# Kernel optimization log

Hardware: AMD Instinct MI355X
Metric: run time of the kernel (lower is better)

Reference implementation:

```python
import jax, jax.numpy as jnp
import numpy as np

N_NODES = 100000
N_EDGES = 3200000
IN_DIM = 64
HID_DIM = 128
OUT_DIM = 2


def setup_inputs() -> dict:
    key = jax.random.key(0)
    k1, k2, k3, k4, k5, k6 = jax.random.split(key, 6)
    x = jax.random.normal(k1, (N_NODES, IN_DIM), dtype=jnp.float32)
    edge_index = jax.random.randint(k2, (2, N_EDGES), 0, N_NODES, dtype=jnp.int64)
    W_gcn = jax.random.normal(k3, (IN_DIM, HID_DIM), dtype=jnp.float32) / np.sqrt(IN_DIM)
    b_gcn = jax.random.normal(k4, (HID_DIM,), dtype=jnp.float32) * 0.02
    W_lin = jax.random.normal(k5, (HID_DIM, OUT_DIM), dtype=jnp.float32) / np.sqrt(HID_DIM)
    b_lin = jax.random.normal(k6, (OUT_DIM,), dtype=jnp.float32) * 0.02
    return {"x": x, "edge_index": edge_index, "W_gcn": W_gcn, "b_gcn": b_gcn,
            "W_lin": W_lin, "b_lin": b_lin}


def reference(x, edge_index, W_gcn, b_gcn, W_lin, b_lin):
    # GCNConv (PyG semantics): add self-loops, symmetric deg^{-1/2} norm,
    # aggregate source->target, then relu, dropout(eval=identity), linear.
    N = x.shape[0]
    loop = jnp.arange(N, dtype=edge_index.dtype)
    src = jnp.concatenate([edge_index[0], loop])  # message sources
    dst = jnp.concatenate([edge_index[1], loop])  # message targets

    h = x @ W_gcn  # [N, HID] - transform before propagate (GCNConv order)

    ones = jnp.ones(dst.shape, dtype=h.dtype)
    deg = jax.ops.segment_sum(ones, dst, num_segments=N)  # in-degree incl. self-loop
    dinv = jnp.where(deg > 0, jax.lax.rsqrt(deg), 0.0)
    norm = dinv[src] * dinv[dst]  # [E+N]

    msg = h[src] * norm[:, None]                      # irregular gather
    agg = jax.ops.segment_sum(msg, dst, num_segments=N)  # irregular scatter-add
    agg = agg + b_gcn

    # relu -> dropout(p=0.5, eval mode => identity) -> linear head
    return jax.nn.relu(agg) @ W_lin + b_lin  # [N, OUT_DIM]
```

## Files before the change

### kernel.cpp

```cpp
#include <hip/hip_runtime.h>
#include <hip/hip_fp16.h>

#define N_NODES 100000
#define N_EDGES 3200000
#define IN_DIM 64
#define HID_DIM 128

#define RNODES 128
#define NRANGE 782
#define PCHUNK 128
#define PCHSZ (N_EDGES / PCHUNK)
#define TCAP 80
#define NLCAP 4608

__global__ __launch_bounds__(512) void part_kernel(const int* __restrict__ src,
                                                   const int* __restrict__ dst,
                                                   int* __restrict__ tmp,
                                                   int* __restrict__ tcnt) {
    __shared__ int cur[NRANGE];
    const int c = blockIdx.x, tid = threadIdx.x;
    for (int i = tid; i < NRANGE; i += 512) cur[i] = 0;
    __syncthreads();
    const int e0 = c * PCHSZ;
    for (int i = tid; i < PCHSZ; i += 512) {
        const int d = dst[e0 + i];
        const int s = src[e0 + i];
        const int r = d >> 7;
        const int pos = atomicAdd(&cur[r], 1);
        if (pos < TCAP)
            tmp[(size_t)(r * PCHUNK + c) * TCAP + pos] = s | ((d & 127) << 17);
    }
    __syncthreads();
    for (int i = tid; i < NRANGE; i += 512)
        tcnt[i * PCHUNK + c] = min(cur[i], TCAP);
}

__global__ __launch_bounds__(256) void degscale_kernel(const int* __restrict__ tmp,
                                                       const int* __restrict__ tcnt,
                                                       const float* __restrict__ x,
                                                       int* __restrict__ degn,
                                                       float* __restrict__ dinv,
                                                       __half* __restrict__ y) {
    __shared__ int   cnt[RNODES];
    __shared__ float dvs[RNODES];
    const int r = blockIdx.x, tid = threadIdx.x;
    if (tid < RNODES) cnt[tid] = 0;
    __syncthreads();
    {
        const int c = tid & 127, half = tid >> 7;
        const int tile = r * PCHUNK + c;
        const int n = tcnt[tile];
        const int* t = tmp + (size_t)tile * TCAP;
        for (int i = half; i < n; i += 2) atomicAdd(&cnt[t[i] >> 17], 1);
    }
    __syncthreads();
    if (tid < RNODES) {
        const int node = r * RNODES + tid;
        const int dg = cnt[tid];
        degn[node] = dg;
        const float dv = rsqrtf((float)dg + 1.0f);
        dvs[tid] = dv;
        if (node < N_NODES) dinv[node] = dv;
    }
    __syncthreads();
    for (int i = tid; i < RNODES * 16; i += 256) {
        const int nl = i >> 4, q = i & 15;
        const int node = r * RNODES + nl;
        if (node < N_NODES) {
            const float4 v = ((const float4*)x)[(size_t)node * 16 + q];
            const float dv = dvs[nl];
            __half2 h0 = __floats2half2_rn(v.x * dv, v.y * dv);
            __half2 h1 = __floats2half2_rn(v.z * dv, v.w * dv);
            uint2 pk;
            pk.x = *(unsigned int*)&h0;
            pk.y = *(unsigned int*)&h1;
            ((uint2*)y)[(size_t)node * 16 + q] = pk;
        }
    }
}

__global__ __launch_bounds__(512) void aggb_kernel(const int* __restrict__ tmp,
                                                   const int* __restrict__ tcnt,
                                                   const int* __restrict__ degn,
                                                   const __half* __restrict__ y,
                                                   __half* __restrict__ agg) {
    __shared__ int nodelist[NLCAP];
    __shared__ int sc[RNODES];
    __shared__ int start[RNODES];
    __shared__ int cur[RNODES];
    const int r = blockIdx.x, tid = threadIdx.x;

    int mydeg = 0;
    if (tid < RNODES) {
        mydeg = degn[r * RNODES + tid];
        sc[tid] = mydeg;
    }
    __syncthreads();
    #pragma unroll
    for (int off = 1; off < RNODES; off <<= 1) {
        int v = 0;
        if (tid < RNODES && tid >= off) v = sc[tid - off];
        __syncthreads();
        if (tid < RNODES) sc[tid] += v;
        __syncthreads();
    }
    if (tid < RNODES) {
        start[tid] = sc[tid] - mydeg;
        cur[tid]   = sc[tid] - mydeg;
    }
    __syncthreads();

    {
        const int c = tid & 127, ph = tid >> 7;
        const int tile = r * PCHUNK + c;
        const int n = tcnt[tile];
        const int* t = tmp + (size_t)tile * TCAP;
        for (int i = ph; i < n; i += 4) {
            const int pk = t[i];
            const int slot = atomicAdd(&cur[pk >> 17], 1);
            if (slot < NLCAP) nodelist[slot] = pk & 0x1FFFF;
        }
    }
    __syncthreads();

    const int g = tid >> 3, lane = tid & 7;
    const uint4* y16 = (const uint4*)y;
    for (int nl = g; nl < RNODES; nl += 64) {
        const int node = r * RNODES + nl;
        if (node >= N_NODES) continue;
        float accf[8];
        {
            const uint4 pk = y16[(size_t)node * 8 + lane];
            const __half2* h = (const __half2*)&pk;
            #pragma unroll
            for (int q = 0; q < 4; ++q) {
                const float2 f = __half22float2(h[q]);
                accf[2*q] = f.x; accf[2*q+1] = f.y;
            }
        }
        const int beg = start[nl], end = sc[nl];
        int j = beg;
        for (; j + 4 <= end; j += 4) {
            const int s0 = nodelist[j];
            const int s1 = nodelist[j + 1];
            const int s2 = nodelist[j + 2];
            const int s3 = nodelist[j + 3];
            const uint4 p0 = y16[(size_t)s0 * 8 + lane];
            const uint4 p1 = y16[(size_t)s1 * 8 + lane];
            const uint4 p2 = y16[(size_t)s2 * 8 + lane];
            const uint4 p3 = y16[(size_t)s3 * 8 + lane];
            const __half2* h0 = (const __half2*)&p0;
            const __half2* h1 = (const __half2*)&p1;
            const __half2* h2 = (const __half2*)&p2;
            const __half2* h3 = (const __half2*)&p3;
            #pragma unroll
            for (int q = 0; q < 4; ++q) {
                float2 f0 = __half22float2(h0[q]);
                float2 f1 = __half22float2(h1[q]);
                float2 f2 = __half22float2(h2[q]);
                float2 f3 = __half22float2(h3[q]);
                accf[2*q]   += (f0.x + f1.x) + (f2.x + f3.x);
                accf[2*q+1] += (f0.y + f1.y) + (f2.y + f3.y);
            }
        }
        for (; j < end; ++j) {
            const int s = nodelist[j];
            const uint4 pk = y16[(size_t)s * 8 + lane];
            const __half2* h = (const __half2*)&pk;
            #pragma unroll
            for (int q = 0; q < 4; ++q) {
                const float2 f = __half22float2(h[q]);
                accf[2*q] += f.x; accf[2*q+1] += f.y;
            }
        }
        uint4 o;
        __half2* oh = (__half2*)&o;
        #pragma unroll
        for (int q = 0; q < 4; ++q)
            oh[q] = __floats2half2_rn(accf[2*q], accf[2*q+1]);
        ((uint4*)agg)[(size_t)node * 8 + lane] = o;
    }
}

#define H_NPB 32
__global__ __launch_bounds__(256) void head_kernel(const __half* __restrict__ agg,
                                                   const float* __restrict__ dinv,
                                                   const float* __restrict__ W,
                                                   const float* __restrict__ b_gcn,
                                                   const float* __restrict__ W_lin,
                                                   const float* __restrict__ b_lin,
                                                   float* __restrict__ out) {
    __shared__ float4 Ws[IN_DIM * HID_DIM / 4];
    __shared__ float  as[H_NPB * IN_DIM];
    const int tid = threadIdx.x;

    const float4* W4 = (const float4*)W;
    #pragma unroll
    for (int i = tid; i < IN_DIM * HID_DIM / 4; i += 256) Ws[i] = W4[i];

    const int node0 = blockIdx.x * H_NPB;
    {
        const uint4 a4 = ((const uint4*)(agg + (size_t)node0 * IN_DIM))[tid];
        const __half2* h = (const __half2*)&a4;
        #pragma unroll
        for (int q = 0; q < 4; ++q) {
            const float2 f = __half22float2(h[q]);
            as[tid * 8 + 2*q]     = f.x;
            as[tid * 8 + 2*q + 1] = f.y;
        }
    }
    __syncthreads();

    const int jq = tid & 31;
    const int ng = tid >> 5;
    const float* arow = as + ng * 4 * IN_DIM;

    float4 a0 = {0,0,0,0}, a1 = {0,0,0,0}, a2 = {0,0,0,0}, a3 = {0,0,0,0};
    for (int k = 0; k < IN_DIM; ++k) {
        const float4 wv = Ws[k * 32 + jq];
        const float v0 = arow[k];
        const float v1 = arow[IN_DIM + k];
        const float v2 = arow[2 * IN_DIM + k];
        const float v3 = arow[3 * IN_DIM + k];
        a0.x += v0*wv.x; a0.y += v0*wv.y; a0.z += v0*wv.z; a0.w += v0*wv.w;
        a1.x += v1*wv.x; a1.y += v1*wv.y; a1.z += v1*wv.z; a1.w += v1*wv.w;
        a2.x += v2*wv.x; a2.y += v2*wv.y; a2.z += v2*wv.z; a2.w += v2*wv.w;
        a3.x += v3*wv.x; a3.y += v3*wv.y; a3.z += v3*wv.z; a3.w += v3*wv.w;
    }

    const float4 bg = ((const float4*)b_gcn)[jq];
    const int c0 = jq * 4;
    const float w00 = W_lin[(c0+0)*2], w01 = W_lin[(c0+0)*2+1];
    const float w10 = W_lin[(c0+1)*2], w11 = W_lin[(c0+1)*2+1];
    const float w20 = W_lin[(c0+2)*2], w21 = W_lin[(c0+2)*2+1];
    const float w30 = W_lin[(c0+3)*2], w31 = W_lin[(c0+3)*2+1];
    const float bl0 = b_lin[0], bl1 = b_lin[1];

    float4 am[4] = {a0, a1, a2, a3};
    #pragma unroll
    for (int m = 0; m < 4; ++m) {
        const int node = node0 + ng * 4 + m;
        const float dv = dinv[node];
        float4 v;
        v.x = fmaxf(am[m].x * dv + bg.x, 0.f);
        v.y = fmaxf(am[m].y * dv + bg.y, 0.f);
        v.z = fmaxf(am[m].z * dv + bg.z, 0.f);
        v.w = fmaxf(am[m].w * dv + bg.w, 0.f);
        float o0 = v.x*w00 + v.y*w10 + v.z*w20 + v.w*w30;
        float o1 = v.x*w01 + v.y*w11 + v.z*w21 + v.w*w31;
        #pragma unroll
        for (int off = 16; off > 0; off >>= 1) {
            o0 += __shfl_down(o0, off, 32);
            o1 += __shfl_down(o1, off, 32);
        }
        if (jq == 0) {
            out[(size_t)node * 2 + 0] = o0 + bl0;
            out[(size_t)node * 2 + 1] = o1 + bl1;
        }
    }
}

extern "C" void kernel_launch(void* const* d_in, const int* in_sizes, int n_in,
                              void* d_out, int out_size, void* d_ws, size_t ws_size,
                              hipStream_t stream) {
    const float* x     = (const float*)d_in[0];
    const int*   ei    = (const int*)  d_in[1];
    const float* W_gcn = (const float*)d_in[2];
    const float* b_gcn = (const float*)d_in[3];
    const float* W_lin = (const float*)d_in[4];
    const float* b_lin = (const float*)d_in[5];
    float* out = (float*)d_out;

    int*    tmp  = (int*)d_ws;
    int*    tcnt = tmp + (size_t)NRANGE * PCHUNK * TCAP;
    int*    degn = tcnt + NRANGE * PCHUNK;
    float*  dinv = (float*)(degn + NRANGE * RNODES);
    __half* y    = (__half*)(dinv + N_NODES);
    __half* agg  = y + (size_t)N_NODES * IN_DIM;

    const int* src = ei;
    const int* dst = ei + N_EDGES;

    part_kernel<<<PCHUNK, 512, 0, stream>>>(src, dst, tmp, tcnt);
    degscale_kernel<<<NRANGE, 256, 0, stream>>>(tmp, tcnt, x, degn, dinv, y);
    aggb_kernel<<<NRANGE, 512, 0, stream>>>(tmp, tcnt, degn, y, agg);
    head_kernel<<<N_NODES / H_NPB, 256, 0, stream>>>(agg, dinv, W_gcn, b_gcn, W_lin, b_lin, out);
}
```

Before: 241.2 us.

## Count degrees with global atomics during partition and widen partition grid

The partition kernel now runs with 256 chunks of 1024 threads, so more CUs are in use, and the per-tile capacity drops to match. It also counts node in-degrees directly with global atomicAdd, which removes the degree pass that re-read the partitioned tiles. The old combined degree-and-scale kernel becomes a flat elementwise scale kernel, plus a small zero kernel for the degree array. The cost is 3.2M random global atomics and an extra launch. The smaller tile cap also raises the chance that edges overflow and get dropped, which would leave the degree counts and the node lists out of step.

```diff
diff --git a/kernel.cpp b/kernel.cpp
--- a/kernel.cpp
+++ b/kernel.cpp
@@ -8,75 +8,56 @@
 
 #define RNODES 128
 #define NRANGE 782
-#define PCHUNK 128
+#define PCHUNK 256
 #define PCHSZ (N_EDGES / PCHUNK)
-#define TCAP 80
+#define TCAP 48
 #define NLCAP 4608
 
-__global__ __launch_bounds__(512) void part_kernel(const int* __restrict__ src,
-                                                   const int* __restrict__ dst,
-                                                   int* __restrict__ tmp,
-                                                   int* __restrict__ tcnt) {
+__global__ __launch_bounds__(256) void zero_kernel(int* __restrict__ degn) {
+    const int i = blockIdx.x * 256 + threadIdx.x;
+    if (i < NRANGE * RNODES) degn[i] = 0;
+}
+
+__global__ __launch_bounds__(1024) void part_kernel(const int* __restrict__ src,
+                                                    const int* __restrict__ dst,
+                                                    int* __restrict__ tmp,
+                                                    int* __restrict__ tcnt,
+                                                    int* __restrict__ degn) {
     __shared__ int cur[NRANGE];
     const int c = blockIdx.x, tid = threadIdx.x;
-    for (int i = tid; i < NRANGE; i += 512) cur[i] = 0;
+    for (int i = tid; i < NRANGE; i += 1024) cur[i] = 0;
     __syncthreads();
     const int e0 = c * PCHSZ;
-    for (int i = tid; i < PCHSZ; i += 512) {
+    for (int i = tid; i < PCHSZ; i += 1024) {
         const int d = dst[e0 + i];
         const int s = src[e0 + i];
+        atomicAdd(&degn[d], 1);
         const int r = d >> 7;
         const int pos = atomicAdd(&cur[r], 1);
         if (pos < TCAP)
             tmp[(size_t)(r * PCHUNK + c) * TCAP + pos] = s | ((d & 127) << 17);
     }
     __syncthreads();
-    for (int i = tid; i < NRANGE; i += 512)
+    for (int i = tid; i < NRANGE; i += 1024)
         tcnt[i * PCHUNK + c] = min(cur[i], TCAP);
 }
 
-__global__ __launch_bounds__(256) void degscale_kernel(const int* __restrict__ tmp,
-                                                       const int* __restrict__ tcnt,
-                                                       const float* __restrict__ x,
-                                                       int* __restrict__ degn,
-                                                       float* __restrict__ dinv,
-                                                       __half* __restrict__ y) {
-    __shared__ int   cnt[RNODES];
-    __shared__ float dvs[RNODES];
-    const int r = blockIdx.x, tid = threadIdx.x;
-    if (tid < RNODES) cnt[tid] = 0;
-    __syncthreads();
-    {
-        const int c = tid & 127, half = tid >> 7;
-        const int tile = r * PCHUNK + c;
-        const int n = tcnt[tile];
-        const int* t = tmp + (size_t)tile * TCAP;
-        for (int i = half; i < n; i += 2) atomicAdd(&cnt[t[i] >> 17], 1);
-    }
-    __syncthreads();
-    if (tid < RNODES) {
-        const int node = r * RNODES + tid;
-        const int dg = cnt[tid];
-        degn[node] = dg;
-        const float dv = rsqrtf((float)dg + 1.0f);
-        dvs[tid] = dv;
-        if (node < N_NODES) dinv[node] = dv;
-    }
-    __syncthreads();
-    for (int i = tid; i < RNODES * 16; i += 256) {
-        const int nl = i >> 4, q = i & 15;
-        const int node = r * RNODES + nl;
-        if (node < N_NODES) {
-            const float4 v = ((const float4*)x)[(size_t)node * 16 + q];
-            const float dv = dvs[nl];
-            __half2 h0 = __floats2half2_rn(v.x * dv, v.y * dv);
-            __half2 h1 = __floats2half2_rn(v.z * dv, v.w * dv);
-            uint2 pk;
-            pk.x = *(unsigned int*)&h0;
-            pk.y = *(unsigned int*)&h1;
-            ((uint2*)y)[(size_t)node * 16 + q] = pk;
-        }
-    }
+__global__ __launch_bounds__(256) void scale_kernel(const int* __restrict__ degn,
+                                                    const float* __restrict__ x,
+                                                    float* __restrict__ dinv,
+                                                    __half* __restrict__ y) {
+    const int i = blockIdx.x * 256 + threadIdx.x;
+    if (i >= N_NODES * 16) return;
+    const int node = i >> 4, q = i & 15;
+    const float dv = rsqrtf((float)degn[node] + 1.0f);
+    if (q == 0) dinv[node] = dv;
+    const float4 v = ((const float4*)x)[i];
+    __half2 h0 = __floats2half2_rn(v.x * dv, v.y * dv);
+    __half2 h1 = __floats2half2_rn(v.z * dv, v.w * dv);
+    uint2 pk;
+    pk.x = *(unsigned int*)&h0;
+    pk.y = *(unsigned int*)&h1;
+    ((uint2*)y)[i] = pk;
 }
 
 __global__ __launch_bounds__(512) void aggb_kernel(const int* __restrict__ tmp,
@@ -111,11 +92,11 @@
     __syncthreads();
 
     {
-        const int c = tid & 127, ph = tid >> 7;
+        const int c = tid & 255, ph = tid >> 8;
         const int tile = r * PCHUNK + c;
         const int n = tcnt[tile];
         const int* t = tmp + (size_t)tile * TCAP;
-        for (int i = ph; i < n; i += 4) {
+        for (int i = ph; i < n; i += 2) {
             const int pk = t[i];
             const int slot = atomicAdd(&cur[pk >> 17], 1);
             if (slot < NLCAP) nodelist[slot] = pk & 0x1FFFF;
@@ -281,8 +262,9 @@
     const int* src = ei;
     const int* dst = ei + N_EDGES;
 
-    part_kernel<<<PCHUNK, 512, 0, stream>>>(src, dst, tmp, tcnt);
-    degscale_kernel<<<NRANGE, 256, 0, stream>>>(tmp, tcnt, x, degn, dinv, y);
+    zero_kernel<<<(NRANGE * RNODES + 255) / 256, 256, 0, stream>>>(degn);
+    part_kernel<<<PCHUNK, 1024, 0, stream>>>(src, dst, tmp, tcnt, degn);
+    scale_kernel<<<(N_NODES * 16) / 256, 256, 0, stream>>>(degn, x, dinv, y);
     aggb_kernel<<<NRANGE, 512, 0, stream>>>(tmp, tcnt, degn, y, agg);
     head_kernel<<<N_NODES / H_NPB, 256, 0, stream>>>(agg, dinv, W_gcn, b_gcn, W_lin, b_lin, out);
 }
```

Result: slower. 323.5 us (+34.1%).
